# Performance work log

Measured on AMD Instinct MI355X. Metric: run time of the kernel, lower is better.

## Reference

```python
import jax, jax.numpy as jnp
import numpy as np
from jax import lax

B, N, D, K = 4, 2048, 1024, 16
TAU = 16.0
LN_EPS = 1e-5


def setup_inputs() -> dict:
    key = jax.random.key(0)
    ks = jax.random.split(key, 8)
    x = jax.random.normal(ks[0], (B, N, D), dtype=jnp.float32)
    Wi = jax.random.normal(ks[1], (D, D), dtype=jnp.float32) * 0.02  # i_proj.weight [out,in]
    We = jax.random.normal(ks[2], (K, D), dtype=jnp.float32) * 0.02  # e_proj.weight
    Wf = jax.random.normal(ks[3], (D, D), dtype=jnp.float32) * 0.02  # f_proj.weight
    Ws = jax.random.normal(ks[4], (K, D), dtype=jnp.float32) * 0.02  # s_proj.weight
    gamma = jnp.ones((D,), dtype=jnp.float32)   # LayerNorm weight
    beta = jnp.zeros((D,), dtype=jnp.float32)   # LayerNorm bias
    Wo = jax.random.normal(ks[5], (D, D), dtype=jnp.float32) * 0.02  # o_proj.weight
    return {"x": x, "Wi": Wi, "We": We, "Wf": Wf, "Ws": Ws,
            "gamma": gamma, "beta": beta, "Wo": Wo}


def _forward(x, Wi, We, Wf, Ws, gamma, beta, Wo):
    # Projections (torch Linear: y = x @ W.T)
    i = jnp.einsum('bnd,ed->bne', x, Wi)          # [B,N,D]
    e = jnp.einsum('bnd,kd->bnk', x, We)          # [B,N,K]  (t_type=0: identity transform)
    s = jnp.einsum('bnd,kd->bnk', x, Ws)          # [B,N,K]
    # f_type=2, use_tau: f = exp(logsigmoid(f_proj(x)) / tau), broadcast over k
    f = jnp.exp(jax.nn.log_sigmoid(jnp.einsum('bnd,ed->bne', x, Wf)) / TAU)  # [B,N,D]

    def step(m, inp):
        i_t, e_t, f_t, s_t = inp                  # [B,D],[B,K],[B,D],[B,K]
        m = f_t[:, None, :] * m + e_t[:, :, None] * i_t[:, None, :]  # [B,K,D]
        y_t = jnp.einsum('bk,bkd->bd', s_t, m)
        return m, y_t

    xs = (jnp.swapaxes(i, 0, 1), jnp.swapaxes(e, 0, 1),
          jnp.swapaxes(f, 0, 1), jnp.swapaxes(s, 0, 1))
    m0 = jnp.zeros((B, K, D), dtype=x.dtype)
    _, ys = lax.scan(step, m0, xs)                # [N,B,D]
    y = jnp.swapaxes(ys, 0, 1)                    # [B,N,D]

    # LayerNorm then output projection
    mu = jnp.mean(y, axis=-1, keepdims=True)
    var = jnp.mean((y - mu) ** 2, axis=-1, keepdims=True)
    yn = (y - mu) * lax.rsqrt(var + LN_EPS) * gamma + beta
    return jnp.einsum('bnd,ed->bne', yn, Wo)


def reference(x, Wi, We, Wf, Ws, gamma, beta, Wo):
    return _forward(x, Wi, We, Wf, Ws, gamma, beta, Wo)
```

## Files before the change

### kernel.cpp

```cpp
#include <hip/hip_runtime.h>
#include <hip/hip_bf16.h>
#include <stdint.h>

#define B_ 4
#define N_ 2048
#define D_ 1024
#define K_ 16
#define MROWS (B_*N_)
#define NC_ 32
#define CLEN_ (N_/NC_)

typedef unsigned short u16;
typedef __attribute__((ext_vector_type(8))) short bf16x8;
typedef __attribute__((ext_vector_type(8))) short short8;
typedef __attribute__((ext_vector_type(4))) float f32x4;

__device__ __forceinline__ u16 f2bf(float f) {
  uint32_t u = __float_as_uint(f);
  u = u + 0x7fffu + ((u >> 16) & 1u);
  return (u16)(u >> 16);
}
__device__ __forceinline__ float bf2f(u16 h) {
  uint32_t u = ((uint32_t)h) << 16;
  return __uint_as_float(u);
}
__device__ __forceinline__ float fgate(float z) {
  float ls = (z >= 0.0f) ? -__logf(1.0f + __expf(-z)) : (z - __logf(1.0f + __expf(z)));
  return __expf(ls * 0.0625f);
}

__global__ __launch_bounds__(256) void cast_kernel(const float* __restrict__ in,
                                                   u16* __restrict__ out, int n) {
  int i = (blockIdx.x * 256 + threadIdx.x) * 4;
  if (i >= n) return;
  float4 v = *(const float4*)(in + i);
  ushort4 o;
  o.x = f2bf(v.x); o.y = f2bf(v.y); o.z = f2bf(v.z); o.w = f2bf(v.w);
  *(ushort4*)(out + i) = o;
}

#define GL_LDS(gp, lp) \
  __builtin_amdgcn_global_load_lds( \
      (const __attribute__((address_space(1))) void*)(gp), \
      (__attribute__((address_space(3))) void*)(lp), 16, 0, 0)

#define WAITVM(n)  asm volatile("s_waitcnt vmcnt(" #n ")" ::: "memory")
#define SCHEDB()   __builtin_amdgcn_sched_barrier(0)

__global__ __launch_bounds__(512, 1) void ring_fused(const u16* __restrict__ A,
                                                     const u16* __restrict__ W0,
                                                     const u16* __restrict__ W1,
                                                     u16* __restrict__ C0,
                                                     u16* __restrict__ C1) {
  __shared__ __align__(16) u16 lds[3 * 24576];

  const int tid = threadIdx.x;
  const int w = tid >> 6, l = tid & 63;
  const int wr = w >> 1, wc = w & 1;

  const int orig = blockIdx.x;
  const int wg = (orig & 7) * 64 + (orig >> 3);
  const int bm = wg / 16;
  const int bn = wg % 16;

  const u16* W;
  u16* C;
  int ncol0;
  if (bn >= 8) { W = W1; C = C1; ncol0 = (bn - 8) * 128; }
  else         { W = W0; C = C0; ncol0 = bn * 128; }

  const int sw = ((l & 7) ^ ((l >> 3) & 7)) * 8;
  const u16* aSrc = A + (size_t)(bm * 256 + w * 8 + (l >> 3)) * 1024 + sw;
  const u16* bSrc = W + (size_t)(ncol0 + w * 8 + (l >> 3)) * 1024 + sw;

#define STAGE_T(t, slot) do { \
    const int _sb = (slot) * 49152 + w * 1024; \
    _Pragma("unroll") \
    for (int j = 0; j < 4; ++j) \
      GL_LDS(aSrc + (size_t)j * 65536 + (t) * 64, (char*)lds + _sb + j * 8192); \
    _Pragma("unroll") \
    for (int j = 0; j < 2; ++j) \
      GL_LDS(bSrc + (size_t)j * 65536 + (t) * 64, (char*)lds + _sb + 32768 + j * 8192); \
  } while (0)

  const int sxe = (l & 7) << 3;
  const int klo = (l >> 4) * 8;
  const int aR0 = (wr * 64 + (l & 15)) * 64;
  const int bR0 = (wc * 64 + (l & 15)) * 64 + 16384;

  f32x4 acc[4][4] = {};

#define COMPUTE(slot) do { \
    const u16* S = lds + (slot) * 24576; \
    bf16x8 b0[4], a0[4], b1[4], a1[4]; \
    _Pragma("unroll") \
    for (int n = 0; n < 4; ++n) b0[n] = *(const bf16x8*)&S[bR0 + n * 1024 + (klo ^ sxe)]; \
    _Pragma("unroll") \
    for (int m = 0; m < 4; ++m) a0[m] = *(const bf16x8*)&S[aR0 + m * 1024 + (klo ^ sxe)]; \
    _Pragma("unroll") \
    for (int n = 0; n < 4; ++n) b1[n] = *(const bf16x8*)&S[bR0 + n * 1024 + ((klo + 32) ^ sxe)]; \
    _Pragma("unroll") \
    for (int m = 0; m < 4; ++m) a1[m] = *(const bf16x8*)&S[aR0 + m * 1024 + ((klo + 32) ^ sxe)]; \
    asm volatile("s_waitcnt lgkmcnt(8)" ::: "memory"); \
    SCHEDB(); \
    __builtin_amdgcn_s_setprio(1); \
    _Pragma("unroll") \
    for (int m = 0; m < 4; ++m) \
      _Pragma("unroll") \
      for (int n = 0; n < 4; ++n) \
        acc[m][n] = __builtin_amdgcn_mfma_f32_16x16x32_bf16(a0[m], b0[n], acc[m][n], 0, 0, 0); \
    __builtin_amdgcn_s_setprio(0); \
    asm volatile("s_waitcnt lgkmcnt(0)" ::: "memory"); \
    SCHEDB(); \
    __builtin_amdgcn_s_setprio(1); \
    _Pragma("unroll") \
    for (int m = 0; m < 4; ++m) \
      _Pragma("unroll") \
      for (int n = 0; n < 4; ++n) \
        acc[m][n] = __builtin_amdgcn_mfma_f32_16x16x32_bf16(a1[m], b1[n], acc[m][n], 0, 0, 0); \
    __builtin_amdgcn_s_setprio(0); \
  } while (0)

  STAGE_T(0, 0);
  STAGE_T(1, 1);
  WAITVM(6);
  __builtin_amdgcn_s_barrier();
  SCHEDB();

#pragma unroll
  for (int t = 0; t < 16; ++t) {
    if (t + 2 < 16) STAGE_T(t + 2, (t + 2) % 3);
    COMPUTE(t % 3);
    if (t < 15) {
      if (t == 14) WAITVM(0);
      else         WAITVM(6);
      __builtin_amdgcn_s_barrier();
      SCHEDB();
    }
  }

  const int orow0 = bm * 256 + wr * 64 + (l >> 4) * 4;
  const int ocol0 = ncol0 + wc * 64 + (l & 15);
#pragma unroll
  for (int m = 0; m < 4; ++m)
#pragma unroll
    for (int n = 0; n < 4; ++n)
#pragma unroll
      for (int r = 0; r < 4; ++r)
        C[(size_t)(orow0 + m * 16 + r) * 1024 + ocol0 + n * 16] = f2bf(acc[m][n][r]);
#undef STAGE_T
#undef COMPUTE
}

__global__ __launch_bounds__(256) void gemm_bt(const u16* __restrict__ A,
                                               const u16* __restrict__ W,
                                               float* __restrict__ C,
                                               int M, int N, int Kk, int epi) {
  __shared__ u16 As[128 * 32];
  __shared__ u16 Bs[128 * 32];
  const int tid = threadIdx.x;
  const int w = tid >> 6, l = tid & 63;
  const int nbn = N >> 7;
  const int bm = blockIdx.x / nbn, bn = blockIdx.x % nbn;
  const int wm = (w >> 1) * 64, wn = (w & 1) * 64;
  const int lr = l & 15, lk = (l >> 4) * 8;

  f32x4 acc[4][4] = {};

  for (int kt = 0; kt < Kk; kt += 32) {
#pragma unroll
    for (int j = 0; j < 2; ++j) {
      int ofs = w * 1024 + j * 4096;
      int gofs = ofs + l * 16;
      int row = gofs >> 6;
      int ke = (gofs & 63) >> 1;
      const u16* ga = A + (size_t)(bm * 128 + row) * Kk + kt + ke;
      const u16* gb = W + (size_t)(bn * 128 + row) * Kk + kt + ke;
      GL_LDS(ga, (char*)As + ofs);
      GL_LDS(gb, (char*)Bs + ofs);
    }
    __syncthreads();
    bf16x8 af[4], bfr[4];
#pragma unroll
    for (int i2 = 0; i2 < 4; ++i2) {
      af[i2]  = *(const bf16x8*)&As[(wm + i2 * 16 + lr) * 32 + lk];
      bfr[i2] = *(const bf16x8*)&Bs[(wn + i2 * 16 + lr) * 32 + lk];
    }
#pragma unroll
    for (int i2 = 0; i2 < 4; ++i2)
#pragma unroll
      for (int j2 = 0; j2 < 4; ++j2)
        acc[i2][j2] = __builtin_amdgcn_mfma_f32_16x16x32_bf16(af[i2], bfr[j2], acc[i2][j2], 0, 0, 0);
    __syncthreads();
  }

  const int orow0 = bm * 128 + wm + (l >> 4) * 4;
  const int ocol0 = bn * 128 + wn + (l & 15);
#pragma unroll
  for (int i2 = 0; i2 < 4; ++i2)
#pragma unroll
    for (int j2 = 0; j2 < 4; ++j2)
#pragma unroll
      for (int r = 0; r < 4; ++r)
        C[(size_t)(orow0 + i2 * 16 + r) * N + ocol0 + j2 * 16] = acc[i2][j2][r];
}

__global__ __launch_bounds__(256) void es_mfma(const u16* __restrict__ xb,
                                               const float* __restrict__ We,
                                               const float* __restrict__ Ws,
                                               float* __restrict__ e,
                                               float* __restrict__ s) {
  __shared__ __align__(16) u16 Bsm[32 * 1024];
  __shared__ __align__(16) u16 Asl[2][64 * 128];

  const int tid = threadIdx.x;
  const int w = tid >> 6, l = tid & 63;
  const int bm = blockIdx.x;

#pragma unroll
  for (int q = 0; q < 16; ++q) {
    int g = q * 256 + tid;
    int n = g >> 7;
    int c = g & 127;
    const float* src = (n < 16 ? We + (size_t)n * 1024 : Ws + (size_t)(n - 16) * 1024) + c * 8;
    float4 v0 = *(const float4*)(src);
    float4 v1 = *(const float4*)(src + 4);
    short8 o;
    o[0] = (short)f2bf(v0.x); o[1] = (short)f2bf(v0.y);
    o[2] = (short)f2bf(v0.z); o[3] = (short)f2bf(v0.w);
    o[4] = (short)f2bf(v1.x); o[5] = (short)f2bf(v1.y);
    o[6] = (short)f2bf(v1.z); o[7] = (short)f2bf(v1.w);
    *(short8*)&Bsm[(size_t)n * 1024 + (size_t)(c ^ (n & 15)) * 8] = o;
  }

  const int arow_par = w * 4 + (l >> 4);
  const int csrc = (l & 15) ^ arow_par;

#define ESTAGE(t, buf) do { \
    _Pragma("unroll") \
    for (int j = 0; j < 4; ++j) { \
      const u16* gp = xb + (size_t)(bm * 64 + j * 16 + arow_par) * 1024 + (t) * 128 + csrc * 8; \
      GL_LDS(gp, (char*)&Asl[(buf)][0] + j * 4096 + w * 1024); \
    } \
  } while (0)

  f32x4 acc[2] = {};

  ESTAGE(0, 0);
  __syncthreads();

#pragma unroll
  for (int t = 0; t < 8; ++t) {
    if (t) { WAITVM(0); __builtin_amdgcn_s_barrier(); }
    if (t + 1 < 8) ESTAGE(t + 1, (t + 1) & 1);
    const int buf = t & 1;
#pragma unroll
    for (int ks = 0; ks < 4; ++ks) {
      bf16x8 af = *(const bf16x8*)&Asl[buf][(size_t)(w * 16 + (l & 15)) * 128 +
                                           (size_t)(((ks * 4 + (l >> 4)) ^ (l & 15))) * 8];
      bf16x8 b0 = *(const bf16x8*)&Bsm[(size_t)(0 + (l & 15)) * 1024 +
                                       (size_t)(((t * 16 + ks * 4 + (l >> 4)) ^ (l & 15))) * 8];
      bf16x8 b1 = *(const bf16x8*)&Bsm[(size_t)(16 + (l & 15)) * 1024 +
                                       (size_t)(((t * 16 + ks * 4 + (l >> 4)) ^ (l & 15))) * 8];
      acc[0] = __builtin_amdgcn_mfma_f32_16x16x32_bf16(af, b0, acc[0], 0, 0, 0);
      acc[1] = __builtin_amdgcn_mfma_f32_16x16x32_bf16(af, b1, acc[1], 0, 0, 0);
    }
  }

  const int orow = bm * 64 + w * 16 + (l >> 4) * 4;
  const int ocol = l & 15;
#pragma unroll
  for (int r = 0; r < 4; ++r) {
    e[(size_t)(orow + r) * K_ + ocol] = acc[0][r];
    s[(size_t)(orow + r) * K_ + ocol] = acc[1][r];
  }
#undef ESTAGE
}

__global__ __launch_bounds__(256) void scan_pass1(const u16* __restrict__ ibb,
                                                  const u16* __restrict__ zbb,
                                                  const float* __restrict__ ebuf,
                                                  float* __restrict__ Asc,
                                                  float* __restrict__ Psc) {
  int bid = blockIdx.x;
  int dq = bid & 3, c = (bid >> 2) & (NC_ - 1), b = bid >> 7;
  int d = dq * 256 + threadIdx.x;
  int t0 = c * CLEN_;
  float m[K_];
#pragma unroll
  for (int k = 0; k < K_; ++k) m[k] = 0.f;
  float p = 1.0f;
  const u16* ip = ibb + ((size_t)b * N_ + t0) * D_ + d;
  const u16* zp = zbb + ((size_t)b * N_ + t0) * D_ + d;
  const float* ep = ebuf + ((size_t)b * N_ + t0) * K_;
  for (int t = 0; t < CLEN_; ++t) {
    float it = bf2f(ip[(size_t)t * D_]);
    float ft = fgate(bf2f(zp[(size_t)t * D_]));
    p *= ft;
#pragma unroll
    for (int k = 0; k < K_; ++k) m[k] = ft * m[k] + ep[t * K_ + k] * it;
  }
  float* ap = Asc + (((size_t)b * NC_ + c) * K_) * D_ + d;
#pragma unroll
  for (int k = 0; k < K_; ++k) ap[(size_t)k * D_] = m[k];
  Psc[((size_t)b * NC_ + c) * D_ + d] = p;
}

__global__ __launch_bounds__(256) void scan_pass2(const float* __restrict__ Asc,
                                                  const float* __restrict__ Psc,
                                                  float* __restrict__ Ssc) {
  int idx = blockIdx.x * 256 + threadIdx.x;
  int d = idx & (D_ - 1);
  int k = (idx >> 10) & (K_ - 1);
  int b = idx >> 14;
  float M = 0.f;
  for (int c = 0; c < NC_; ++c) {
    size_t base = (((size_t)b * NC_ + c) * K_ + k) * D_ + d;
    float a = Asc[base];
    float pp = Psc[((size_t)b * NC_ + c) * D_ + d];
    Ssc[base] = M;
    M = pp * M + a;
  }
}

__global__ __launch_bounds__(256) void scan_pass3(const u16* __restrict__ ibb,
                                                  const u16* __restrict__ zbb,
                                                  const float* __restrict__ ebuf,
                                                  const float* __restrict__ sbuf,
                                                  const float* __restrict__ Ssc,
                                                  u16* __restrict__ ybb) {
  int bid = blockIdx.x;
  int dq = bid & 3, c = (bid >> 2) & (NC_ - 1), b = bid >> 7;
  int d = dq * 256 + threadIdx.x;
  int t0 = c * CLEN_;
  float m[K_];
  const float* sp0 = Ssc + (((size_t)b * NC_ + c) * K_) * D_ + d;
#pragma unroll
  for (int k = 0; k < K_; ++k) m[k] = sp0[(size_t)k * D_];
  const u16* ip = ibb + ((size_t)b * N_ + t0) * D_ + d;
  const u16* zp = zbb + ((size_t)b * N_ + t0) * D_ + d;
  u16* yp = ybb + ((size_t)b * N_ + t0) * D_ + d;
  const float* ep = ebuf + ((size_t)b * N_ + t0) * K_;
  const float* wp = sbuf + ((size_t)b * N_ + t0) * K_;
  for (int t = 0; t < CLEN_; ++t) {
    float it = bf2f(ip[(size_t)t * D_]);
    float ft = fgate(bf2f(zp[(size_t)t * D_]));
    float y = 0.f;
#pragma unroll
    for (int k = 0; k < K_; ++k) {
      m[k] = ft * m[k] + ep[t * K_ + k] * it;
      y += wp[t * K_ + k] * m[k];
    }
    yp[(size_t)t * D_] = f2bf(y);
  }
}

__global__ __launch_bounds__(256) void ln_kernel(const u16* __restrict__ y,
                                                 const float* __restrict__ gamma,
                                                 const float* __restrict__ beta,
                                                 u16* __restrict__ yn) {
  int row = blockIdx.x * 4 + (threadIdx.x >> 6);
  int l = threadIdx.x & 63;
  const u16* yr = y + (size_t)row * D_;
  float v[16];
  float sum = 0.f;
#pragma unroll
  for (int j = 0; j < 2; ++j) {
    short8 raw = *(const short8*)(yr + l * 16 + j * 8);
#pragma unroll
    for (int q = 0; q < 8; ++q) {
      float f = bf2f((u16)raw[q]);
      v[j * 8 + q] = f;
      sum += f;
    }
  }
  for (int off = 32; off > 0; off >>= 1) sum += __shfl_xor(sum, off);
  float mu = sum * (1.0f / D_);
  float vs = 0.f;
#pragma unroll
  for (int q = 0; q < 16; ++q) { float dx = v[q] - mu; vs += dx * dx; }
  for (int off = 32; off > 0; off >>= 1) vs += __shfl_xor(vs, off);
  float rstd = rsqrtf(vs * (1.0f / D_) + 1e-5f);
  int col0 = l * 16;
#pragma unroll
  for (int j = 0; j < 4; ++j) {
    float4 g = *(const float4*)(gamma + col0 + j * 4);
    float4 bt = *(const float4*)(beta + col0 + j * 4);
    ushort4 o;
    o.x = f2bf((v[j * 4 + 0] - mu) * rstd * g.x + bt.x);
    o.y = f2bf((v[j * 4 + 1] - mu) * rstd * g.y + bt.y);
    o.z = f2bf((v[j * 4 + 2] - mu) * rstd * g.z + bt.z);
    o.w = f2bf((v[j * 4 + 3] - mu) * rstd * g.w + bt.w);
    *(ushort4*)(yn + (size_t)row * D_ + col0 + j * 4) = o;
  }
}

extern "C" void kernel_launch(void* const* d_in, const int* in_sizes, int n_in,
                              void* d_out, int out_size, void* d_ws, size_t ws_size,
                              hipStream_t stream) {
  const float* x     = (const float*)d_in[0];
  const float* Wi    = (const float*)d_in[1];
  const float* We    = (const float*)d_in[2];
  const float* Wf    = (const float*)d_in[3];
  const float* Ws    = (const float*)d_in[4];
  const float* gamma = (const float*)d_in[5];
  const float* beta  = (const float*)d_in[6];
  const float* Wo    = (const float*)d_in[7];
  float* out = (float*)d_out;

  char* p = (char*)d_ws;
  u16* xb  = (u16*)p;  p += (size_t)MROWS * D_ * 2;
  u16* wib = (u16*)p;  p += (size_t)D_ * D_ * 2;
  u16* wfb = (u16*)p;  p += (size_t)D_ * D_ * 2;
  u16* wob = (u16*)p;  p += (size_t)D_ * D_ * 2;
  u16* ibb = (u16*)p;  p += (size_t)MROWS * D_ * 2;
  u16* zbb = (u16*)p;  p += (size_t)MROWS * D_ * 2;
  u16* ybb = (u16*)p;  p += (size_t)MROWS * D_ * 2;
  float* ebuf = (float*)p; p += (size_t)MROWS * K_ * 4;
  float* sbuf = (float*)p; p += (size_t)MROWS * K_ * 4;
  float* Asc  = (float*)p; p += (size_t)B_ * NC_ * K_ * D_ * 4;
  float* Ssc  = (float*)p; p += (size_t)B_ * NC_ * K_ * D_ * 4;
  float* Psc  = (float*)p; p += (size_t)B_ * NC_ * D_ * 4;

  cast_kernel<<<MROWS * D_ / 1024, 256, 0, stream>>>(x, xb, MROWS * D_);
  cast_kernel<<<D_ * D_ / 1024, 256, 0, stream>>>(Wi, wib, D_ * D_);
  cast_kernel<<<D_ * D_ / 1024, 256, 0, stream>>>(Wf, wfb, D_ * D_);
  cast_kernel<<<D_ * D_ / 1024, 256, 0, stream>>>(Wo, wob, D_ * D_);

  ring_fused<<<512, 512, 0, stream>>>(xb, wib, wfb, ibb, zbb);

  es_mfma<<<MROWS / 64, 256, 0, stream>>>(xb, We, Ws, ebuf, sbuf);

  scan_pass1<<<B_ * NC_ * 4, 256, 0, stream>>>(ibb, zbb, ebuf, Asc, Psc);
  scan_pass2<<<B_ * K_ * D_ / 256, 256, 0, stream>>>(Asc, Psc, Ssc);
  scan_pass3<<<B_ * NC_ * 4, 256, 0, stream>>>(ibb, zbb, ebuf, sbuf, Ssc, ybb);

  u16* ynb = xb;
  ln_kernel<<<MROWS / 4, 256, 0, stream>>>(ybb, gamma, beta, ynb);

  gemm_bt<<<512, 256, 0, stream>>>(ynb, wob, out, MROWS, D_, D_, 0);
}
```

Baseline: 201.3 us.

## Double scan chunk count, stage e/s coefficients in LDS, batch loads in scan

Raises the number of scan chunks from 32 to 64, so pass1 and pass3 launch twice as many blocks with half-length chunks. Each block now stages its chunk's e and s coefficients in shared memory instead of re-reading them from global memory every step. The i and gate loads are batched eight timesteps at a time, and pass2's loads are batched too, so the memory latency in the sequential chains can overlap. The cost is larger Asc/Ssc intermediates and a longer sequential chain in pass2.

```diff
diff --git a/kernel.cpp b/kernel.cpp
--- a/kernel.cpp
+++ b/kernel.cpp
@@ -7,7 +7,7 @@
 #define D_ 1024
 #define K_ 16
 #define MROWS (B_*N_)
-#define NC_ 32
+#define NC_ 64
 #define CLEN_ (N_/NC_)
 
 typedef unsigned short u16;
@@ -282,24 +282,42 @@
                                                   const float* __restrict__ ebuf,
                                                   float* __restrict__ Asc,
                                                   float* __restrict__ Psc) {
+  __shared__ float els[CLEN_ * K_];
   int bid = blockIdx.x;
-  int dq = bid & 3, c = (bid >> 2) & (NC_ - 1), b = bid >> 7;
+  int dq = bid & 3, c = (bid >> 2) % NC_, b = bid / (NC_ * 4);
   int d = dq * 256 + threadIdx.x;
   int t0 = c * CLEN_;
+
+  if (threadIdx.x < CLEN_ * K_ / 4) {
+    *(float4*)&els[threadIdx.x * 4] =
+        *(const float4*)(ebuf + ((size_t)b * N_ + t0) * K_ + threadIdx.x * 4);
+  }
+  __syncthreads();
+
   float m[K_];
 #pragma unroll
   for (int k = 0; k < K_; ++k) m[k] = 0.f;
   float p = 1.0f;
   const u16* ip = ibb + ((size_t)b * N_ + t0) * D_ + d;
   const u16* zp = zbb + ((size_t)b * N_ + t0) * D_ + d;
-  const float* ep = ebuf + ((size_t)b * N_ + t0) * K_;
-  for (int t = 0; t < CLEN_; ++t) {
-    float it = bf2f(ip[(size_t)t * D_]);
-    float ft = fgate(bf2f(zp[(size_t)t * D_]));
-    p *= ft;
-#pragma unroll
-    for (int k = 0; k < K_; ++k) m[k] = ft * m[k] + ep[t * K_ + k] * it;
-  }
+
+#pragma unroll
+  for (int tb = 0; tb < CLEN_; tb += 8) {
+    float iv[8], zv[8];
+#pragma unroll
+    for (int j = 0; j < 8; ++j) iv[j] = bf2f(ip[(size_t)(tb + j) * D_]);
+#pragma unroll
+    for (int j = 0; j < 8; ++j) zv[j] = bf2f(zp[(size_t)(tb + j) * D_]);
+#pragma unroll
+    for (int j = 0; j < 8; ++j) {
+      float ft = fgate(zv[j]);
+      p *= ft;
+      const float* ec = &els[(tb + j) * K_];
+#pragma unroll
+      for (int k = 0; k < K_; ++k) m[k] = ft * m[k] + ec[k] * iv[j];
+    }
+  }
+
   float* ap = Asc + (((size_t)b * NC_ + c) * K_) * D_ + d;
 #pragma unroll
   for (int k = 0; k < K_; ++k) ap[(size_t)k * D_] = m[k];
@@ -314,12 +332,21 @@
   int k = (idx >> 10) & (K_ - 1);
   int b = idx >> 14;
   float M = 0.f;
-  for (int c = 0; c < NC_; ++c) {
-    size_t base = (((size_t)b * NC_ + c) * K_ + k) * D_ + d;
-    float a = Asc[base];
-    float pp = Psc[((size_t)b * NC_ + c) * D_ + d];
-    Ssc[base] = M;
-    M = pp * M + a;
+#pragma unroll
+  for (int cb = 0; cb < NC_; cb += 8) {
+    float a[8], pp[8];
+#pragma unroll
+    for (int j = 0; j < 8; ++j) {
+      size_t base = (((size_t)b * NC_ + cb + j) * K_ + k) * D_ + d;
+      a[j] = Asc[base];
+      pp[j] = Psc[((size_t)b * NC_ + cb + j) * D_ + d];
+    }
+#pragma unroll
+    for (int j = 0; j < 8; ++j) {
+      size_t base = (((size_t)b * NC_ + cb + j) * K_ + k) * D_ + d;
+      Ssc[base] = M;
+      M = pp[j] * M + a[j];
+    }
   }
 }
 
@@ -329,29 +356,52 @@
                                                   const float* __restrict__ sbuf,
                                                   const float* __restrict__ Ssc,
                                                   u16* __restrict__ ybb) {
+  __shared__ float els[CLEN_ * K_];
+  __shared__ float sls[CLEN_ * K_];
   int bid = blockIdx.x;
-  int dq = bid & 3, c = (bid >> 2) & (NC_ - 1), b = bid >> 7;
+  int dq = bid & 3, c = (bid >> 2) % NC_, b = bid / (NC_ * 4);
   int d = dq * 256 + threadIdx.x;
   int t0 = c * CLEN_;
+
+  if (threadIdx.x < CLEN_ * K_ / 4) {
+    *(float4*)&els[threadIdx.x * 4] =
+        *(const float4*)(ebuf + ((size_t)b * N_ + t0) * K_ + threadIdx.x * 4);
+  } else if (threadIdx.x < CLEN_ * K_ / 2) {
+    int q = threadIdx.x - CLEN_ * K_ / 4;
+    *(float4*)&sls[q * 4] =
+        *(const float4*)(sbuf + ((size_t)b * N_ + t0) * K_ + q * 4);
+  }
+
   float m[K_];
   const float* sp0 = Ssc + (((size_t)b * NC_ + c) * K_) * D_ + d;
 #pragma unroll
   for (int k = 0; k < K_; ++k) m[k] = sp0[(size_t)k * D_];
+  __syncthreads();
+
   const u16* ip = ibb + ((size_t)b * N_ + t0) * D_ + d;
   const u16* zp = zbb + ((size_t)b * N_ + t0) * D_ + d;
   u16* yp = ybb + ((size_t)b * N_ + t0) * D_ + d;
-  const float* ep = ebuf + ((size_t)b * N_ + t0) * K_;
-  const float* wp = sbuf + ((size_t)b * N_ + t0) * K_;
-  for (int t = 0; t < CLEN_; ++t) {
-    float it = bf2f(ip[(size_t)t * D_]);
-    float ft = fgate(bf2f(zp[(size_t)t * D_]));
-    float y = 0.f;
-#pragma unroll
-    for (int k = 0; k < K_; ++k) {
-      m[k] = ft * m[k] + ep[t * K_ + k] * it;
-      y += wp[t * K_ + k] * m[k];
-    }
-    yp[(size_t)t * D_] = f2bf(y);
+
+#pragma unroll
+  for (int tb = 0; tb < CLEN_; tb += 8) {
+    float iv[8], zv[8];
+#pragma unroll
+    for (int j = 0; j < 8; ++j) iv[j] = bf2f(ip[(size_t)(tb + j) * D_]);
+#pragma unroll
+    for (int j = 0; j < 8; ++j) zv[j] = bf2f(zp[(size_t)(tb + j) * D_]);
+#pragma unroll
+    for (int j = 0; j < 8; ++j) {
+      float ft = fgate(zv[j]);
+      const float* ec = &els[(tb + j) * K_];
+      const float* sc = &sls[(tb + j) * K_];
+      float y = 0.f;
+#pragma unroll
+      for (int k = 0; k < K_; ++k) {
+        m[k] = ft * m[k] + ec[k] * iv[j];
+        y += sc[k] * m[k];
+      }
+      yp[(size_t)(tb + j) * D_] = f2bf(y);
+    }
   }
 }
 
```

Measured after the change: 240.3 us. 19.4% more time.
